# Kernel optimization log

Hardware: AMD Instinct MI355X
Metric: run time of the kernel (lower is better)

Reference implementation:

```python
import jax, jax.numpy as jnp
import numpy as np

B, N, DIM = 8, 512, 768
H, DH = 12, 64
INNER = H * DH
MLP = 3072
DEPTH = 4
EPS = 1e-5
LS = 0.1  # LayerScale init_eps for depth <= 18


def _ln(x, scale):
    # flax LayerNorm(use_bias=False): (x-mean)/sqrt(var+eps) * scale
    mu = jnp.mean(x, axis=-1, keepdims=True)
    var = jnp.mean(jnp.square(x - mu), axis=-1, keepdims=True)
    return (x - mu) * jax.lax.rsqrt(var + EPS) * scale


def setup_inputs() -> dict:
    key = jax.random.key(0)
    ks = jax.random.split(key, 13)
    s = 0.02
    inp = {
        "x": jax.random.normal(ks[0], (B, N, DIM), jnp.float32),
        "ln1": jnp.ones((DEPTH, DIM), jnp.float32),
        "Wq": jax.random.normal(ks[1], (DEPTH, DIM, INNER), jnp.float32) * s,
        "Wkv": jax.random.normal(ks[2], (DEPTH, DIM, 2 * INNER), jnp.float32) * s,
        "mix_pre": jax.random.normal(ks[3], (DEPTH, H, H), jnp.float32) * 0.1,
        "mix_post": jax.random.normal(ks[4], (DEPTH, H, H), jnp.float32) * 0.1,
        "Wo": jax.random.normal(ks[5], (DEPTH, INNER, DIM), jnp.float32) * s,
        "bo": jnp.zeros((DEPTH, DIM), jnp.float32),
        "ln2": jnp.ones((DEPTH, DIM), jnp.float32),
        "W1": jax.random.normal(ks[6], (DEPTH, DIM, MLP), jnp.float32) * s,
        "b1": jnp.zeros((DEPTH, MLP), jnp.float32),
        "W2": jax.random.normal(ks[7], (DEPTH, MLP, DIM), jnp.float32) * s,
        "b2": jnp.zeros((DEPTH, DIM), jnp.float32),
    }
    return inp


def _block(x, p):
    ln1, Wq, Wkv, mp, mq, Wo, bo, ln2, W1, b1, W2, b2 = p
    scale = DH ** -0.5
    h = _ln(x, ln1)
    q = h @ Wq                                  # [b,n,inner]
    kv = h @ Wkv
    k, v = jnp.split(kv, 2, axis=-1)
    def to_heads(t):
        return t.reshape(B, N, H, DH).transpose(0, 2, 1, 3)  # b h n d
    q, k, v = to_heads(q), to_heads(k), to_heads(v)
    dots = jnp.einsum('bhid,bhjd->bhij', q, k) * scale
    dots = jnp.einsum('bhij,hg->bgij', dots, mp)   # talking-heads pre-softmax
    attn = jax.nn.softmax(dots, axis=-1)
    attn = jnp.einsum('bhij,hg->bgij', attn, mq)   # talking-heads post-softmax
    o = jnp.einsum('bhij,bhjd->bhid', attn, v)
    o = o.transpose(0, 2, 1, 3).reshape(B, N, INNER)
    x = (o @ Wo + bo) * LS + x
    h2 = _ln(x, ln2)
    x = ((jax.nn.gelu(h2 @ W1 + b1) @ W2) + b2) * LS + x
    return x, None


def reference(x, ln1, Wq, Wkv, mix_pre, mix_post, Wo, bo, ln2, W1, b1, W2, b2):
    params = (ln1, Wq, Wkv, mix_pre, mix_post, Wo, bo, ln2, W1, b1, W2, b2)
    out, _ = jax.lax.scan(_block, x, params)
    return out
```

## Files before the change

kernel.cpp:

```cpp
#include <hip/hip_runtime.h>


#define LSCALE 0.1f

typedef __bf16 bf16;
typedef __bf16 bf16x8 __attribute__((ext_vector_type(8)));
typedef __bf16 bf16x4 __attribute__((ext_vector_type(4)));
typedef unsigned short ushort4v __attribute__((ext_vector_type(4)));
typedef float  f32x4  __attribute__((ext_vector_type(4)));

__device__ __forceinline__ void g2l16(const void* g, void* l) {
    __builtin_amdgcn_global_load_lds(
        (const __attribute__((address_space(1))) void*)g,
        (__attribute__((address_space(3))) void*)l, 16, 0, 0);
}

template<int EPI>
__global__ __launch_bounds__(256, 2)
void gemm_bt(const bf16* __restrict__ A, int lda, long saz1, long saz2,
             const bf16* __restrict__ Bt, int ldb, long sbz1, long sbz2,
             void* __restrict__ Cv, int ldc, long scz1, long scz2,
             int M, int N, int K, int zmod,
             const float* __restrict__ bias, float scale)
{
    __shared__ __align__(16) char smem[35840];
    bf16* As = (bf16*)smem;
    bf16* Bs = (bf16*)(smem + 16384);
    bf16* Cs = (bf16*)smem;

    const int z  = blockIdx.z;
    const int z1 = z / zmod, z2 = z - z1 * zmod;
    const bf16* Ab = A  + saz1 * (long)z1 + saz2 * (long)z2;
    const bf16* Bb = Bt + sbz1 * (long)z1 + sbz2 * (long)z2;

    const int m0 = blockIdx.x * 128, n0 = blockIdx.y * 128;
    const int tid = threadIdx.x, w = tid >> 6, l = tid & 63;
    const int wr = (w >> 1) * 64, wc = (w & 1) * 64;
    const int lr = l & 15, lq = l >> 4;
    const int srow = l >> 2, scol8 = (l & 3) * 8;

    f32x4 acc[4][4];
#pragma unroll
    for (int i = 0; i < 4; i++)
#pragma unroll
        for (int j = 0; j < 4; j++)
#pragma unroll
            for (int r = 0; r < 4; r++) acc[i][j][r] = 0.f;

    for (int k0 = 0; k0 < K; k0 += 64) {
        const bf16* Ag = Ab + (long)(m0 + w * 32) * lda + k0;
        const bf16* Bg = Bb + (long)(n0 + w * 32) * ldb + k0;
        g2l16(Ag + (long)srow * lda + scol8,             As + w * 1024);
        g2l16(Ag + (long)(srow + 16) * lda + scol8,      As + w * 1024 + 512);
        g2l16(Ag + (long)srow * lda + 32 + scol8,        As + 4096 + w * 1024);
        g2l16(Ag + (long)(srow + 16) * lda + 32 + scol8, As + 4096 + w * 1024 + 512);
        g2l16(Bg + (long)srow * ldb + scol8,             Bs + w * 1024);
        g2l16(Bg + (long)(srow + 16) * ldb + scol8,      Bs + w * 1024 + 512);
        g2l16(Bg + (long)srow * ldb + 32 + scol8,        Bs + 4096 + w * 1024);
        g2l16(Bg + (long)(srow + 16) * ldb + 32 + scol8, Bs + 4096 + w * 1024 + 512);
        __syncthreads();

#pragma unroll
        for (int hh = 0; hh < 2; hh++) {
            bf16x8 fa[4], fb[4];
#pragma unroll
            for (int i = 0; i < 4; i++)
                fa[i] = *(const bf16x8*)(As + hh * 4096 + (wr + i * 16 + lr) * 32 + lq * 8);
#pragma unroll
            for (int i = 0; i < 4; i++)
                fb[i] = *(const bf16x8*)(Bs + hh * 4096 + (wc + i * 16 + lr) * 32 + lq * 8);
#pragma unroll
            for (int mi = 0; mi < 4; mi++)
#pragma unroll
                for (int ni = 0; ni < 4; ni++)
                    acc[mi][ni] = __builtin_amdgcn_mfma_f32_16x16x32_bf16(
                        fa[mi], fb[ni], acc[mi][ni], 0, 0, 0);
        }
        __syncthreads();
    }

#pragma unroll
    for (int ni = 0; ni < 4; ni++) {
        const int col = wc + ni * 16 + lr;
        float bv = 0.f;
        if (EPI == 1) bv = bias[n0 + col];
#pragma unroll
        for (int mi = 0; mi < 4; mi++) {
#pragma unroll
            for (int r = 0; r < 4; r++) {
                const int row = wr + mi * 16 + lq * 4 + r;
                float v = acc[mi][ni][r];
                if (EPI == 0) {
                    v *= scale;
                } else if (EPI == 1) {
                    const float xx = v + bv;
                    const float u  = 0.7978845608f * (xx + 0.044715f * xx * xx * xx);
                    const float th = 1.f - 2.f / (__expf(2.f * u) + 1.f);
                    v = 0.5f * xx * (1.f + th);
                }
                Cs[row * 136 + col] = (bf16)v;
            }
        }
    }
    __syncthreads();

    const long cb = scz1 * (long)z1 + scz2 * (long)z2;
    const int rrow = tid >> 4, cg = tid & 15;
#pragma unroll
    for (int p = 0; p < 8; p++) {
        const int row = p * 16 + rrow;
        const bf16x8 v = *(const bf16x8*)(Cs + row * 136 + cg * 8);
        *(bf16x8*)((bf16*)Cv + cb + (long)(m0 + row) * ldc + n0 + cg * 8) = v;
    }
}

__global__ __launch_bounds__(256, 4)
void gemm_av(const bf16* __restrict__ S, const bf16* __restrict__ qkvc,
             bf16* __restrict__ oc)
{
    __shared__ __align__(16) bf16 As[64 * 32];
    __shared__ __align__(16) bf16 Bst[64 * 40];

    const int z = blockIdx.y, b = z / 12, g = z - b * 12;
    const bf16* Ab = S + (long)z * 262144;
    const bf16* Bb = qkvc + (long)b * 1179648 + 1536 + g * 64;
    bf16* Cb = oc + (long)b * 1179648 + g * 64;

    const int i0 = blockIdx.x * 64;
    const int tid = threadIdx.x, w = tid >> 6, l = tid & 63;
    const int lr = l & 15, lq = l >> 4;
    const int srow = l >> 2, scol8 = (l & 3) * 8;
    const int kp = tid >> 4, dq = tid & 15;
    const int kcol = ((((kp >> 2) ^ ((dq >> 1) & 3)) << 3) | ((kp & 3) << 1));

    f32x4 acc[4];
#pragma unroll
    for (int j = 0; j < 4; j++)
#pragma unroll
        for (int r = 0; r < 4; r++) acc[j][r] = 0.f;

    unsigned short* Bw = (unsigned short*)Bst;

    for (int k0 = 0; k0 < 512; k0 += 32) {
        const bf16* Ag = Ab + (long)(i0 + w * 16) * 512 + k0;
        g2l16(Ag + (long)srow * 512 + scol8, As + w * 512);

        const bf16* Bg = Bb + (long)(k0 + 2 * kp) * 2304 + dq * 4;
        ushort4v u0 = *(const ushort4v*)(Bg);
        ushort4v u1 = *(const ushort4v*)(Bg + 2304);
#pragma unroll
        for (int r = 0; r < 4; r++) {
            unsigned p = (unsigned)u0[r] | ((unsigned)u1[r] << 16);
            *(unsigned*)(Bw + (dq * 4 + r) * 40 + kcol) = p;
        }
        __syncthreads();

        bf16x8 fa = *(const bf16x8*)(As + (w * 16 + lr) * 32 + lq * 8);
        bf16x8 fb[4];
#pragma unroll
        for (int i = 0; i < 4; i++) {
            const int d = i * 16 + lr;
            fb[i] = *(const bf16x8*)(Bst + d * 40 + ((lq ^ ((d >> 3) & 3)) << 3));
        }
#pragma unroll
        for (int ni = 0; ni < 4; ni++)
            acc[ni] = __builtin_amdgcn_mfma_f32_16x16x32_bf16(
                fa, fb[ni], acc[ni], 0, 0, 0);
        __syncthreads();
    }

#pragma unroll
    for (int ni = 0; ni < 4; ni++) {
        const int gc = ni * 16 + lr;
#pragma unroll
        for (int r = 0; r < 4; r++) {
            const int gr = i0 + w * 16 + lq * 4 + r;
            Cb[(long)gr * 2304 + gc] = (bf16)acc[ni][r];
        }
    }
}

__global__ __launch_bounds__(256)
void tconv_k(const float* __restrict__ in, bf16* __restrict__ out,
             int K, int N)
{
    __shared__ float t[32][33];
    const int n0 = blockIdx.x * 32, k0 = blockIdx.y * 32;
    const int x = threadIdx.x, y = threadIdx.y;
#pragma unroll
    for (int yy = 0; yy < 4; yy++)
        t[y + yy * 8][x] = in[(long)(k0 + y + yy * 8) * N + n0 + x];
    __syncthreads();
#pragma unroll
    for (int yy = 0; yy < 4; yy++)
        out[(long)(n0 + y + yy * 8) * K + k0 + x] = (bf16)t[x][y + yy * 8];
}

__global__ __launch_bounds__(256)
void tconv_all(const float* __restrict__ Wq, const float* __restrict__ Wkv,
               const float* __restrict__ Wo, const float* __restrict__ W1,
               const float* __restrict__ W2, bf16* __restrict__ WtAll)
{
    __shared__ float st[64][65];
    const int L = blockIdx.y;
    bf16* WtL = WtAll + (long)L * 7077888;
    int bx = blockIdx.x;
    const float* src; bf16* dst; int K, N, ntn;
    if (bx < 144) {
        src = Wq + (long)L * 589824;   dst = WtL;            K = 768;  N = 768;  ntn = 12;
    } else if (bx < 432) {
        bx -= 144;
        src = Wkv + (long)L * 1179648; dst = WtL + 589824;   K = 768;  N = 1536; ntn = 24;
    } else if (bx < 576) {
        bx -= 432;
        src = Wo + (long)L * 589824;   dst = WtL + 1769472;  K = 768;  N = 768;  ntn = 12;
    } else if (bx < 1152) {
        bx -= 576;
        src = W1 + (long)L * 2359296;  dst = WtL + 2359296;  K = 768;  N = 3072; ntn = 48;
    } else {
        bx -= 1152;
        src = W2 + (long)L * 2359296;  dst = WtL + 4718592;  K = 3072; N = 768;  ntn = 12;
    }
    const int n0 = (bx % ntn) * 64, k0 = (bx / ntn) * 64;
    const int t = threadIdx.x;
    const int r = t >> 4, c4 = (t & 15) * 4;
#pragma unroll
    for (int rr = 0; rr < 4; rr++) {
        const f32x4 v = *(const f32x4*)(src + (long)(k0 + r + rr * 16) * N + n0 + c4);
        st[r + rr * 16][c4 + 0] = v[0];
        st[r + rr * 16][c4 + 1] = v[1];
        st[r + rr * 16][c4 + 2] = v[2];
        st[r + rr * 16][c4 + 3] = v[3];
    }
    __syncthreads();
    const int kc = (t & 7) * 8;
#pragma unroll
    for (int p = 0; p < 2; p++) {
        const int n = p * 32 + (t >> 3);
        bf16x8 o;
#pragma unroll
        for (int e = 0; e < 8; e++) o[e] = (bf16)st[kc + e][n];
        *(bf16x8*)(dst + (long)(n0 + n) * K + k0 + kc) = o;
    }
}

__global__ __launch_bounds__(256)
void lnres_k(float* __restrict__ xf, const bf16* __restrict__ P0,
             const bf16* __restrict__ P1, const float* __restrict__ bias,
             const float* __restrict__ gam, bf16* __restrict__ out,
             const float* __restrict__ src)
{
    const int row = blockIdx.x, t = threadIdx.x;
    float* xr = xf + (long)row * 768;
    float v[3];
#pragma unroll
    for (int i = 0; i < 3; i++) {
        const int c = t + i * 256;
        float xv;
        if (src) {
            xv = src[(long)row * 768 + c];
            xr[c] = xv;
        } else if (P0) {
            xv = xr[c] + LSCALE * ((float)P0[(long)row * 768 + c] +
                                   (float)P1[(long)row * 768 + c] + bias[c]);
            xr[c] = xv;
        } else {
            xv = xr[c];
        }
        v[i] = xv;
    }
    float s  = v[0] + v[1] + v[2];
    float ss = v[0] * v[0] + v[1] * v[1] + v[2] * v[2];
#pragma unroll
    for (int off = 32; off; off >>= 1) {
        s  += __shfl_xor(s, off);
        ss += __shfl_xor(ss, off);
    }
    __shared__ float ps[4], pss[4];
    const int wv = t >> 6, l = t & 63;
    if (l == 0) { ps[wv] = s; pss[wv] = ss; }
    __syncthreads();
    s  = ps[0] + ps[1] + ps[2] + ps[3];
    ss = pss[0] + pss[1] + pss[2] + pss[3];
    const float mu = s * (1.f / 768.f);
    const float rs = rsqrtf(ss * (1.f / 768.f) - mu * mu + 1e-5f);
    bf16* orow = out + (long)row * 768;
#pragma unroll
    for (int i = 0; i < 3; i++) {
        const int c = t + i * 256;
        orow[c] = (bf16)((v[i] - mu) * rs * gam[c]);
    }
}

__global__ __launch_bounds__(256)
void outres_k(const float* __restrict__ xf, const bf16* __restrict__ P0,
              const bf16* __restrict__ P1, const float* __restrict__ bias,
              float* __restrict__ out)
{
    const long i4 = ((long)blockIdx.x * 256 + threadIdx.x) * 4;
    const int c = (int)(i4 % 768);
    const f32x4 xv = *(const f32x4*)(xf + i4);
    const bf16x4 p0 = *(const bf16x4*)(P0 + i4);
    const bf16x4 p1 = *(const bf16x4*)(P1 + i4);
    const f32x4 bv = *(const f32x4*)(bias + c);
    f32x4 o;
#pragma unroll
    for (int e = 0; e < 4; e++)
        o[e] = xv[e] + LSCALE * ((float)p0[e] + (float)p1[e] + bv[e]);
    *(f32x4*)(out + i4) = o;
}

__global__ __launch_bounds__(256)
void mixsm_k(bf16* __restrict__ S, const float* __restrict__ mp,
             const float* __restrict__ mq)
{
    __shared__ float buf[12][512];
    __shared__ float rds[12];
    const int b = blockIdx.y, i = blockIdx.x, t = threadIdx.x;
    bf16* Sb = S + ((long)b * 12 * 512 + i) * 512;

    float s0[12], s1[12];
#pragma unroll
    for (int h = 0; h < 12; h++) {
        union { unsigned u; bf16 v[2]; } p;
        p.u = *(const unsigned*)(Sb + (long)h * 262144 + 2 * t);
        s0[h] = (float)p.v[0];
        s1[h] = (float)p.v[1];
    }
#pragma unroll
    for (int g = 0; g < 12; g++) {
        float a0 = 0.f, a1 = 0.f;
#pragma unroll
        for (int h = 0; h < 12; h++) {
            const float m = mp[h * 12 + g];
            a0 += s0[h] * m;
            a1 += s1[h] * m;
        }
        *(float2*)(&buf[g][2 * t]) = make_float2(a0, a1);
    }
    __syncthreads();

    const int wv = t >> 6, l = t & 63;
    for (int g = wv; g < 12; g += 4) {
        float mx = -3.0e38f;
#pragma unroll
        for (int k = 0; k < 8; k++) mx = fmaxf(mx, buf[g][l + 64 * k]);
#pragma unroll
        for (int off = 32; off; off >>= 1) mx = fmaxf(mx, __shfl_xor(mx, off));
        float sm = 0.f;
#pragma unroll
        for (int k = 0; k < 8; k++) {
            const float e = __expf(buf[g][l + 64 * k] - mx);
            buf[g][l + 64 * k] = e;
            sm += e;
        }
#pragma unroll
        for (int off = 32; off; off >>= 1) sm += __shfl_xor(sm, off);
        if (l == 0) rds[g] = 1.f / sm;
    }
    __syncthreads();

    float e0[12], e1[12];
#pragma unroll
    for (int h = 0; h < 12; h++) {
        const float2 ee = *(const float2*)(&buf[h][2 * t]);
        const float rd = rds[h];
        e0[h] = ee.x * rd;
        e1[h] = ee.y * rd;
    }
#pragma unroll
    for (int g = 0; g < 12; g++) {
        float a0 = 0.f, a1 = 0.f;
#pragma unroll
        for (int h = 0; h < 12; h++) {
            const float m = mq[h * 12 + g];
            a0 += e0[h] * m;
            a1 += e1[h] * m;
        }
        union { unsigned u; bf16 v[2]; } p;
        p.v[0] = (bf16)a0;
        p.v[1] = (bf16)a1;
        *(unsigned*)(Sb + (long)g * 262144 + 2 * t) = p.u;
    }
}

extern "C" void kernel_launch(void* const* d_in, const int* in_sizes, int n_in,
                              void* d_out, int out_size, void* d_ws, size_t ws_size,
                              hipStream_t stream)
{
    (void)in_sizes; (void)n_in; (void)out_size;
    const float* x   = (const float*)d_in[0];
    const float* ln1 = (const float*)d_in[1];
    const float* Wq  = (const float*)d_in[2];
    const float* Wkv = (const float*)d_in[3];
    const float* mp  = (const float*)d_in[4];
    const float* mq  = (const float*)d_in[5];
    const float* Wo  = (const float*)d_in[6];
    const float* bo  = (const float*)d_in[7];
    const float* ln2 = (const float*)d_in[8];
    const float* W1  = (const float*)d_in[9];
    const float* b1  = (const float*)d_in[10];
    const float* W2  = (const float*)d_in[11];
    const float* b2  = (const float*)d_in[12];

    char* ws = (char*)d_ws;
    float* xf  = (float*)(ws);
    bf16* h    = (bf16*)(ws + 12582912);
    bf16* qkv  = (bf16*)(ws + 18874368);
    bf16* S    = (bf16*)(ws + 37748736);
    bf16* mid  = S;
    bf16* P0   = h;
    bf16* P1w2 = qkv;
    bf16* P1wo = S;
    const long P1W2_OFF = 3145728;
    const long P1WO_OFF = 12582912;

    const dim3 tb(32, 8);

    if (ws_size >= 144703488ull) {
        bf16* WtAll = (bf16*)(ws + 88080384);

        tconv_all<<<dim3(1728, 4), 256, 0, stream>>>(Wq, Wkv, Wo, W1, W2, WtAll);

        for (int L = 0; L < 4; L++) {
            bf16* WtL = WtAll + (long)L * 7077888;

            if (L == 0)
                lnres_k<<<4096, 256, 0, stream>>>(xf, nullptr, nullptr, nullptr,
                                                  ln1 + L * 768, h, x);
            else
                lnres_k<<<4096, 256, 0, stream>>>(xf, P0, P1w2, b2 + (L - 1) * 768,
                                                  ln1 + L * 768, h, nullptr);

            gemm_bt<0><<<dim3(32, 18, 1), 256, 0, stream>>>(
                h, 768, 0, 0, WtL, 768, 0, 0,
                qkv, 2304, 0, 0, 4096, 2304, 768, 1, nullptr, 1.f);

            gemm_bt<0><<<dim3(4, 4, 96), 256, 0, stream>>>(
                qkv,       2304, 1179648, 64,
                qkv + 768, 2304, 1179648, 64,
                S,          512, 3145728, 262144,
                512, 512, 64, 12, nullptr, 0.125f);

            mixsm_k<<<dim3(512, 8), 256, 0, stream>>>(S, mp + L * 144, mq + L * 144);

            gemm_av<<<dim3(8, 96), 256, 0, stream>>>(S, qkv, qkv);

            gemm_bt<4><<<dim3(32, 6, 2), 256, 0, stream>>>(
                qkv, 2304, 0, 384, WtL + 1769472, 768, 0, 384,
                P0, 768, 0, P1WO_OFF, 4096, 768, 384, 2, nullptr, 1.f);

            lnres_k<<<4096, 256, 0, stream>>>(xf, P0, P1wo, bo + L * 768,
                                              ln2 + L * 768, h, nullptr);

            gemm_bt<1><<<dim3(32, 24, 1), 256, 0, stream>>>(
                h, 768, 0, 0, WtL + 2359296, 768, 0, 0,
                mid, 3072, 0, 0, 4096, 3072, 768, 1, b1 + L * 3072, 1.f);

            gemm_bt<4><<<dim3(32, 6, 2), 256, 0, stream>>>(
                mid, 3072, 0, 1536, WtL + 4718592, 3072, 0, 1536,
                P0, 768, 0, P1W2_OFF, 4096, 768, 1536, 2, nullptr, 1.f);
        }
    } else {
        bf16* Wt = (bf16*)(ws + 62914560);

        for (int L = 0; L < 4; L++) {
            tconv_k<<<dim3(24, 24), tb, 0, stream>>>(Wq + (long)L * 589824, Wt, 768, 768);
            tconv_k<<<dim3(48, 24), tb, 0, stream>>>(Wkv + (long)L * 1179648, Wt + 589824, 768, 1536);

            if (L == 0)
                lnres_k<<<4096, 256, 0, stream>>>(xf, nullptr, nullptr, nullptr,
                                                  ln1 + L * 768, h, x);
            else
                lnres_k<<<4096, 256, 0, stream>>>(xf, P0, P1w2, b2 + (L - 1) * 768,
                                                  ln1 + L * 768, h, nullptr);

            gemm_bt<0><<<dim3(32, 18, 1), 256, 0, stream>>>(
                h, 768, 0, 0, Wt, 768, 0, 0,
                qkv, 2304, 0, 0, 4096, 2304, 768, 1, nullptr, 1.f);

            for (int c = 0; c < 2; c++) {
                const long qb = (long)c * 4718592;
                gemm_bt<0><<<dim3(4, 4, 48), 256, 0, stream>>>(
                    qkv + qb,       2304, 1179648, 64,
                    qkv + 768 + qb, 2304, 1179648, 64,
                    S,               512, 3145728, 262144,
                    512, 512, 64, 12, nullptr, 0.125f);

                mixsm_k<<<dim3(512, 4), 256, 0, stream>>>(S, mp + L * 144, mq + L * 144);

                gemm_av<<<dim3(8, 48), 256, 0, stream>>>(S, qkv + qb, qkv + qb);
            }

            tconv_k<<<dim3(24, 24), tb, 0, stream>>>(Wo + (long)L * 589824, Wt, 768, 768);
            gemm_bt<4><<<dim3(32, 6, 2), 256, 0, stream>>>(
                qkv, 2304, 0, 384, Wt, 768, 0, 384,
                P0, 768, 0, P1WO_OFF, 4096, 768, 384, 2, nullptr, 1.f);

            lnres_k<<<4096, 256, 0, stream>>>(xf, P0, P1wo, bo + L * 768,
                                              ln2 + L * 768, h, nullptr);

            tconv_k<<<dim3(96, 24), tb, 0, stream>>>(W1 + (long)L * 2359296, Wt, 768, 3072);
            gemm_bt<1><<<dim3(32, 24, 1), 256, 0, stream>>>(
                h, 768, 0, 0, Wt, 768, 0, 0,
                mid, 3072, 0, 0, 4096, 3072, 768, 1, b1 + L * 3072, 1.f);

            tconv_k<<<dim3(24, 96), tb, 0, stream>>>(W2 + (long)L * 2359296, Wt, 3072, 768);
            gemm_bt<4><<<dim3(32, 6, 2), 256, 0, stream>>>(
                mid, 3072, 0, 1536, Wt, 3072, 0, 1536,
                P0, 768, 0, P1W2_OFF, 4096, 768, 1536, 2, nullptr, 1.f);
        }
    }

    outres_k<<<3072, 256, 0, stream>>>(xf, P0, P1w2, b2 + 3 * 768, (float*)d_out);
}
```

Measured before the change: 890.5 us.

## Write attention output in head-planar layout and retile weight transpose kernel

```diff
diff --git a/kernel.cpp b/kernel.cpp
--- a/kernel.cpp
+++ b/kernel.cpp
@@ -15,7 +15,7 @@
         (__attribute__((address_space(3))) void*)l, 16, 0, 0);
 }
 
-template<int EPI>
+template<int EPI, bool PLANA = false>
 __global__ __launch_bounds__(256, 2)
 void gemm_bt(const bf16* __restrict__ A, int lda, long saz1, long saz2,
              const bf16* __restrict__ Bt, int ldb, long sbz1, long sbz2,
@@ -39,6 +39,10 @@
     const int lr = l & 15, lq = l >> 4;
     const int srow = l >> 2, scol8 = (l & 3) * 8;
 
+    long abase = 0;
+    if constexpr (PLANA)
+        abase = (long)(m0 >> 9) * 393216 + (long)((m0 & 511) + w * 32) * 64;
+
     f32x4 acc[4][4];
 #pragma unroll
     for (int i = 0; i < 4; i++)
@@ -48,12 +52,20 @@
             for (int r = 0; r < 4; r++) acc[i][j][r] = 0.f;
 
     for (int k0 = 0; k0 < K; k0 += 64) {
-        const bf16* Ag = Ab + (long)(m0 + w * 32) * lda + k0;
+        const bf16* Ag;
+        int ldaa;
+        if constexpr (PLANA) {
+            Ag = Ab + abase + ((long)(k0 >> 6)) * 32768;
+            ldaa = 64;
+        } else {
+            Ag = Ab + (long)(m0 + w * 32) * lda + k0;
+            ldaa = lda;
+        }
         const bf16* Bg = Bb + (long)(n0 + w * 32) * ldb + k0;
-        g2l16(Ag + (long)srow * lda + scol8,             As + w * 1024);
-        g2l16(Ag + (long)(srow + 16) * lda + scol8,      As + w * 1024 + 512);
-        g2l16(Ag + (long)srow * lda + 32 + scol8,        As + 4096 + w * 1024);
-        g2l16(Ag + (long)(srow + 16) * lda + 32 + scol8, As + 4096 + w * 1024 + 512);
+        g2l16(Ag + (long)srow * ldaa + scol8,             As + w * 1024);
+        g2l16(Ag + (long)(srow + 16) * ldaa + scol8,      As + w * 1024 + 512);
+        g2l16(Ag + (long)srow * ldaa + 32 + scol8,        As + 4096 + w * 1024);
+        g2l16(Ag + (long)(srow + 16) * ldaa + 32 + scol8, As + 4096 + w * 1024 + 512);
         g2l16(Bg + (long)srow * ldb + scol8,             Bs + w * 1024);
         g2l16(Bg + (long)(srow + 16) * ldb + scol8,      Bs + w * 1024 + 512);
         g2l16(Bg + (long)srow * ldb + 32 + scol8,        Bs + 4096 + w * 1024);
@@ -114,17 +126,19 @@
     }
 }
 
+template<int PLANO>
 __global__ __launch_bounds__(256, 4)
 void gemm_av(const bf16* __restrict__ S, const bf16* __restrict__ qkvc,
              bf16* __restrict__ oc)
 {
-    __shared__ __align__(16) bf16 As[64 * 32];
-    __shared__ __align__(16) bf16 Bst[64 * 40];
+    __shared__ __align__(16) char av_smem[9728];
+    bf16* As  = (bf16*)av_smem;
+    bf16* Bst = (bf16*)(av_smem + 4096);
+    bf16* Cs  = (bf16*)av_smem;
 
     const int z = blockIdx.y, b = z / 12, g = z - b * 12;
     const bf16* Ab = S + (long)z * 262144;
     const bf16* Bb = qkvc + (long)b * 1179648 + 1536 + g * 64;
-    bf16* Cb = oc + (long)b * 1179648 + g * 64;
 
     const int i0 = blockIdx.x * 64;
     const int tid = threadIdx.x, w = tid >> 6, l = tid & 63;
@@ -169,13 +183,27 @@
         __syncthreads();
     }
 
-#pragma unroll
-    for (int ni = 0; ni < 4; ni++) {
-        const int gc = ni * 16 + lr;
-#pragma unroll
-        for (int r = 0; r < 4; r++) {
-            const int gr = i0 + w * 16 + lq * 4 + r;
-            Cb[(long)gr * 2304 + gc] = (bf16)acc[ni][r];
+    if constexpr (PLANO) {
+#pragma unroll
+        for (int ni = 0; ni < 4; ni++)
+#pragma unroll
+            for (int r = 0; r < 4; r++)
+                Cs[(w * 16 + lq * 4 + r) * 68 + ni * 16 + lr] = (bf16)acc[ni][r];
+        __syncthreads();
+        const int rr = tid >> 2, c16 = (tid & 3) * 16;
+        bf16* orow = oc + ((long)z * 512 + i0 + rr) * 64 + c16;
+        *(bf16x8*)(orow)     = *(const bf16x8*)(Cs + rr * 68 + c16);
+        *(bf16x8*)(orow + 8) = *(const bf16x8*)(Cs + rr * 68 + c16 + 8);
+    } else {
+        bf16* Cb = oc + (long)b * 1179648 + g * 64;
+#pragma unroll
+        for (int ni = 0; ni < 4; ni++) {
+            const int gc = ni * 16 + lr;
+#pragma unroll
+            for (int r = 0; r < 4; r++) {
+                const int gr = i0 + w * 16 + lq * 4 + r;
+                Cb[(long)gr * 2304 + gc] = (bf16)acc[ni][r];
+            }
         }
     }
 }
@@ -201,46 +229,47 @@
                const float* __restrict__ Wo, const float* __restrict__ W1,
                const float* __restrict__ W2, bf16* __restrict__ WtAll)
 {
-    __shared__ float st[64][65];
+    __shared__ float st[128][65];
     const int L = blockIdx.y;
     bf16* WtL = WtAll + (long)L * 7077888;
     int bx = blockIdx.x;
     const float* src; bf16* dst; int K, N, ntn;
-    if (bx < 144) {
+    if (bx < 72) {
         src = Wq + (long)L * 589824;   dst = WtL;            K = 768;  N = 768;  ntn = 12;
-    } else if (bx < 432) {
-        bx -= 144;
+    } else if (bx < 216) {
+        bx -= 72;
         src = Wkv + (long)L * 1179648; dst = WtL + 589824;   K = 768;  N = 1536; ntn = 24;
+    } else if (bx < 288) {
+        bx -= 216;
+        src = Wo + (long)L * 589824;   dst = WtL + 1769472;  K = 768;  N = 768;  ntn = 12;
     } else if (bx < 576) {
-        bx -= 432;
-        src = Wo + (long)L * 589824;   dst = WtL + 1769472;  K = 768;  N = 768;  ntn = 12;
-    } else if (bx < 1152) {
-        bx -= 576;
+        bx -= 288;
         src = W1 + (long)L * 2359296;  dst = WtL + 2359296;  K = 768;  N = 3072; ntn = 48;
     } else {
-        bx -= 1152;
+        bx -= 576;
         src = W2 + (long)L * 2359296;  dst = WtL + 4718592;  K = 3072; N = 768;  ntn = 12;
     }
-    const int n0 = (bx % ntn) * 64, k0 = (bx / ntn) * 64;
+    const int n0 = (bx % ntn) * 64, k0 = (bx / ntn) * 128;
     const int t = threadIdx.x;
-    const int r = t >> 4, c4 = (t & 15) * 4;
-#pragma unroll
-    for (int rr = 0; rr < 4; rr++) {
-        const f32x4 v = *(const f32x4*)(src + (long)(k0 + r + rr * 16) * N + n0 + c4);
-        st[r + rr * 16][c4 + 0] = v[0];
-        st[r + rr * 16][c4 + 1] = v[1];
-        st[r + rr * 16][c4 + 2] = v[2];
-        st[r + rr * 16][c4 + 3] = v[3];
-    }
+    const int rr = t >> 1, cb = (t & 1) * 32;
+    f32x4 v[8];
+#pragma unroll
+    for (int q = 0; q < 8; q++)
+        v[q] = *(const f32x4*)(src + (long)(k0 + rr) * N + n0 + cb + 4 * q);
+#pragma unroll
+    for (int q = 0; q < 8; q++)
+#pragma unroll
+        for (int j = 0; j < 4; j++)
+            st[rr][cb + 4 * q + j] = v[q][j];
     __syncthreads();
-    const int kc = (t & 7) * 8;
-#pragma unroll
-    for (int p = 0; p < 2; p++) {
-        const int n = p * 32 + (t >> 3);
+    const int kb = (t & 15) * 8;
+#pragma unroll
+    for (int p = 0; p < 4; p++) {
+        const int n = p * 16 + (t >> 4);
         bf16x8 o;
 #pragma unroll
-        for (int e = 0; e < 8; e++) o[e] = (bf16)st[kc + e][n];
-        *(bf16x8*)(dst + (long)(n0 + n) * K + k0 + kc) = o;
+        for (int e = 0; e < 8; e++) o[e] = (bf16)st[kb + e][n];
+        *(bf16x8*)(dst + (long)(n0 + n) * K + k0 + kb) = o;
     }
 }
 
@@ -417,10 +446,11 @@
 
     const dim3 tb(32, 8);
 
-    if (ws_size >= 144703488ull) {
+    if (ws_size >= 150994944ull) {
         bf16* WtAll = (bf16*)(ws + 88080384);
-
-        tconv_all<<<dim3(1728, 4), 256, 0, stream>>>(Wq, Wkv, Wo, W1, W2, WtAll);
+        bf16* oP    = (bf16*)(ws + 144703488);
+
+        tconv_all<<<dim3(864, 4), 256, 0, stream>>>(Wq, Wkv, Wo, W1, W2, WtAll);
 
         for (int L = 0; L < 4; L++) {
             bf16* WtL = WtAll + (long)L * 7077888;
@@ -444,10 +474,10 @@
 
             mixsm_k<<<dim3(512, 8), 256, 0, stream>>>(S, mp + L * 144, mq + L * 144);
 
-            gemm_av<<<dim3(8, 96), 256, 0, stream>>>(S, qkv, qkv);
-
-            gemm_bt<4><<<dim3(32, 6, 2), 256, 0, stream>>>(
-                qkv, 2304, 0, 384, WtL + 1769472, 768, 0, 384,
+            gemm_av<1><<<dim3(8, 96), 256, 0, stream>>>(S, qkv, oP);
+
+            gemm_bt<4, true><<<dim3(32, 6, 2), 256, 0, stream>>>(
+                oP, 64, 0, 196608, WtL + 1769472, 768, 0, 384,
                 P0, 768, 0, P1WO_OFF, 4096, 768, 384, 2, nullptr, 1.f);
 
             lnres_k<<<4096, 256, 0, stream>>>(xf, P0, P1wo, bo + L * 768,
@@ -489,7 +519,7 @@
 
                 mixsm_k<<<dim3(512, 4), 256, 0, stream>>>(S, mp + L * 144, mq + L * 144);
 
-                gemm_av<<<dim3(8, 48), 256, 0, stream>>>(S, qkv + qb, qkv + qb);
+                gemm_av<0><<<dim3(8, 48), 256, 0, stream>>>(S, qkv + qb, qkv + qb);
             }
 
             tconv_k<<<dim3(24, 24), tb, 0, stream>>>(Wo + (long)L * 589824, Wt, 768, 768);
```

Result: no change. 902.1 us (+1.3%).
